# Performance work log

Hardware: AMD Instinct MI355X
Metric: run time of the kernel (lower is better)

Reference implementation:

```python
import jax, jax.numpy as jnp
import numpy as np

# model dims (DeepSeekV2-Lite-like, reduced expert count)
H = 2048      # hidden_dim
NH = 16       # num_heads
NOPE = 128    # qk_nope_head_dim
ROPE = 64     # qk_rope_head_dim (interleaved rotary)
VD = 128      # v_head_dim
QL = 1536     # q_lora_rank
KVL = 512     # kv_lora_rank
E = 8         # num routed experts
TOPK = 2      # num_experts_per_token
MI = 512      # moe_intermediate_dim
SH_I = 2 * MI # num_shared_experts * moe_intermediate_dim
B = 1
S = 2048
T = B * S
EPS = 1e-6
MOE_SCALE = 1.0  # gating_scaling_factor


def setup_inputs() -> dict:
    key = jax.random.key(0)
    ks = jax.random.split(key, 16)
    def w(k, shape):
        return jax.random.normal(k, shape, dtype=jnp.float32) * 0.02
    # interleaved rotary tables: one angle per (even,odd) pair
    half = ROPE // 2
    pos = jnp.arange(S, dtype=jnp.float32)
    inv_freq = 1.0 / (10000.0 ** (jnp.arange(half, dtype=jnp.float32) * 2.0 / ROPE))
    ang = pos[:, None] * inv_freq[None, :]              # [S, half]
    sin = jnp.tile(jnp.sin(ang), (B, 1))                # [T, half]
    cos = jnp.tile(jnp.cos(ang), (B, 1))
    return {
        "x": jax.random.normal(ks[0], (T, H), jnp.float32),
        "skip": jax.random.normal(ks[1], (T, H), jnp.float32),
        "rotary_sin": sin,
        "rotary_cos": cos,
        "ln1_w": jnp.ones((H,), jnp.float32),
        "ln2_w": jnp.ones((H,), jnp.float32),
        "w_qa": w(ks[2], (QL, H)),
        "qa_norm_w": jnp.ones((QL,), jnp.float32),
        "w_qb": w(ks[3], (NH * (NOPE + ROPE), QL)),
        "w_kva": w(ks[4], (KVL + ROPE, H)),
        "kva_norm_w": jnp.ones((KVL,), jnp.float32),
        "w_kb": w(ks[5], (NH * NOPE, KVL)),
        "w_vb": w(ks[6], (NH * VD, KVL)),
        "w_o": w(ks[7], (H, NH * VD)),
        "gate_w": w(ks[8], (E, H)),
        "moe_up_w": w(ks[9], (E, 2 * MI, H)),
        "moe_down_w": w(ks[10], (E, H, MI)),
        "shared_up_w": w(ks[11], (2 * SH_I, H)),
        "shared_down_w": w(ks[12], (H, SH_I)),
        "batch": B,
    }


def _rms(v, w):
    return v * jax.lax.rsqrt(jnp.mean(v * v, axis=-1, keepdims=True) + EPS) * w


def _rope_interleaved(v, sin, cos):
    # v: [T, nh, ROPE]; sin/cos: [T, ROPE//2]; rotate (even, odd) pairs
    x1, x2 = v[..., 0::2], v[..., 1::2]
    s, c = sin[:, None, :], cos[:, None, :]
    o1 = x1 * c - x2 * s
    o2 = x1 * s + x2 * c
    return jnp.stack([o1, o2], axis=-1).reshape(v.shape)


def reference(x, skip, rotary_sin, rotary_cos, ln1_w, ln2_w, w_qa, qa_norm_w,
              w_qb, w_kva, kva_norm_w, w_kb, w_vb, w_o, gate_w,
              moe_up_w, moe_down_w, shared_up_w, shared_down_w, batch):
    Tt = x.shape[0]
    Sq = Tt // batch
    # SkipRMSNorm #1
    x1 = x + skip
    n1 = _rms(x1, ln1_w)
    # ---- MLA attention (prefill path, decoding_batches=0) ----
    qa = _rms(n1 @ w_qa.T, qa_norm_w)                               # [T, QL]
    q = (qa @ w_qb.T).reshape(Tt, NH, NOPE + ROPE)
    q_nope, q_pe = q[..., :NOPE], q[..., NOPE:]
    q_pe = _rope_interleaved(q_pe, rotary_sin, rotary_cos)
    kv = n1 @ w_kva.T                                               # [T, KVL+ROPE]
    ckv = _rms(kv[:, :KVL], kva_norm_w)
    k_pe = _rope_interleaved(kv[:, KVL:][:, None, :], rotary_sin, rotary_cos)  # [T,1,ROPE]
    k_nope = (ckv @ w_kb.T).reshape(Tt, NH, NOPE)
    v = (ckv @ w_vb.T).reshape(Tt, NH, VD)
    qf = jnp.concatenate([q_nope, q_pe], -1).reshape(batch, Sq, NH, NOPE + ROPE)
    kf = jnp.concatenate([k_nope, jnp.broadcast_to(k_pe, (Tt, NH, ROPE))], -1)
    kf = kf.reshape(batch, Sq, NH, NOPE + ROPE)
    vf = v.reshape(batch, Sq, NH, VD)
    scale = 1.0 / np.sqrt(NOPE + ROPE)
    scores = jnp.einsum('bqhd,bkhd->bhqk', qf, kf) * scale
    causal = jnp.tril(jnp.ones((Sq, Sq), bool))
    scores = jnp.where(causal[None, None], scores, jnp.float32(-1e30))
    p = jax.nn.softmax(scores, axis=-1)
    o = jnp.einsum('bhqk,bkhd->bqhd', p, vf).reshape(Tt, NH * VD)
    attn = o @ w_o.T
    # SkipRMSNorm #2
    x2 = x1 + attn
    n2 = _rms(x2, ln2_w)
    # ---- MoE FFN: softmax gate, greedy top-k, normalized probs ----
    probs = jax.nn.softmax(n2 @ gate_w.T, axis=-1)                  # [T, E]
    tv, ti = jax.lax.top_k(probs, TOPK)
    tv = tv / jnp.sum(tv, axis=-1, keepdims=True) * MOE_SCALE
    routed = jnp.zeros_like(n2)
    for e in range(E):  # fixed small expert count; masked dense dispatch
        we = jnp.sum(tv * (ti == e), axis=-1)                       # [T]
        h = n2 @ moe_up_w[e].T                                      # [T, 2*MI]
        h = jax.nn.silu(h[:, :MI]) * h[:, MI:]
        routed = routed + we[:, None] * (h @ moe_down_w[e].T)
    # shared experts (dense swiglu MLP)
    hs = n2 @ shared_up_w.T
    hs = jax.nn.silu(hs[:, :SH_I]) * hs[:, SH_I:]
    ffn = routed + hs @ shared_down_w.T
    return (x2, ffn)
```

## Files before the change

kernel.cpp:

```cpp
#include <hip/hip_runtime.h>
#include <hip/hip_bf16.h>

#define H 2048
#define NH 16
#define NOPE 128
#define ROPE_D 64
#define DQK 192
#define VD 128
#define QL 1536
#define KVL 512
#define NE 8
#define MI_D 512
#define SHI 1024
#define EPS 1e-6f
#define MAXA 5120

typedef unsigned short bfu;
typedef short bf16x8 __attribute__((ext_vector_type(8)));
typedef float f32x4 __attribute__((ext_vector_type(4)));

#define MFMA16(a, b, c) __builtin_amdgcn_mfma_f32_16x16x32_bf16(a, b, c, 0, 0, 0)

#define BAR_PLAIN()   asm volatile("s_barrier" ::: "memory")
#define BAR_LGKM0()   asm volatile("s_waitcnt lgkmcnt(0)\n\ts_barrier" ::: "memory")
#define BAR_VM4()     asm volatile("s_waitcnt vmcnt(4)\n\ts_barrier" ::: "memory")
#define BAR_VM0()     asm volatile("s_waitcnt vmcnt(0)\n\ts_barrier" ::: "memory")

__device__ __forceinline__ float bf2f(bfu u) {
    union { unsigned int i; float f; } w; w.i = ((unsigned int)u) << 16; return w.f;
}
__device__ __forceinline__ bfu f2bf(float f) {
    union { float f; unsigned int i; } u; u.f = f;
    return (bfu)((u.i + 0x7fffu + ((u.i >> 16) & 1u)) >> 16);
}

__device__ __forceinline__ void async16(const bfu* g, bfu* l) {
    __builtin_amdgcn_global_load_lds((const __attribute__((address_space(1))) void*)g,
                                     (__attribute__((address_space(3))) void*)l, 16, 0, 0);
}

__device__ __forceinline__ float blk_sum(float v) {
    __shared__ float sb[4];
    for (int o = 32; o > 0; o >>= 1) v += __shfl_down(v, o, 64);
    int lane = threadIdx.x & 63, w = threadIdx.x >> 6;
    __syncthreads();
    if (lane == 0) sb[w] = v;
    __syncthreads();
    return sb[0] + sb[1] + sb[2] + sb[3];
}

template<int MODE>
__global__ __launch_bounds__(256) void gemm_mfma(const bfu* __restrict__ A, const bfu* __restrict__ B,
                                                 void* __restrict__ Cv, void* __restrict__ Cv2,
                                                 int M, int N, int K, int ldm3,
                                                 const int* __restrict__ aidx,
                                                 const int* __restrict__ eid, long bstride) {
    __shared__ bfu sA[3][128 * 32];
    __shared__ bfu sB[3][128 * 32];
    const int tid = threadIdx.x;
    const int lane = tid & 63, w = tid >> 6;
    const int quad = lane >> 4, li = lane & 15;
    const int m0 = blockIdx.y * 128, n0 = blockIdx.x * 128;
    const bfu* Bp = B + (eid ? (size_t)eid[blockIdx.y] * bstride : 0);

    const int l4 = lane >> 2;
    const int lg = lane & 3;
    const int kc = lg ^ ((lane >> 3) & 3);
    int r0 = m0 + w * 32 + l4, r1 = r0 + 16;
    if (aidx) { r0 = aidx[r0]; r1 = aidx[r1]; }
    const bfu* gA0 = A + (size_t)r0 * K + kc * 8;
    const bfu* gA1 = A + (size_t)r1 * K + kc * 8;
    const bfu* gB0 = Bp + (size_t)(n0 + w * 32 + l4) * K + kc * 8;
    const bfu* gB1 = gB0 + (size_t)16 * K;
    const int oA0 = (w * 32) * 32, oA1 = (w * 32 + 16) * 32;

    const int wm = (w >> 1) * 64, wn = (w & 1) * 64;
    const int fg = (quad ^ ((li >> 1) & 3)) * 8;
    int oa[4], ob[4];
#pragma unroll
    for (int t4 = 0; t4 < 4; ++t4) {
        oa[t4] = (wm + t4 * 16 + li) * 32 + fg;
        ob[t4] = (wn + t4 * 16 + li) * 32 + fg;
    }
    f32x4 acc[4][4];
#pragma unroll
    for (int i = 0; i < 4; ++i)
#pragma unroll
        for (int j = 0; j < 4; ++j) acc[i][j] = (f32x4){0.f, 0.f, 0.f, 0.f};

    const int nb = K / 32;
    async16(gA0, &sA[0][oA0]); async16(gA1, &sA[0][oA1]);
    async16(gB0, &sB[0][oA0]); async16(gB1, &sB[0][oA1]);
    async16(gA0 + 32, &sA[1][oA0]); async16(gA1 + 32, &sA[1][oA1]);
    async16(gB0 + 32, &sB[1][oA0]); async16(gB1 + 32, &sB[1][oA1]);

    int cur = 0;
    for (int it = 0; it < nb; ++it) {
        if (it < nb - 1) { BAR_VM4(); } else { BAR_VM0(); }
        bf16x8 av[4], bv[4];
#pragma unroll
        for (int t4 = 0; t4 < 4; ++t4) av[t4] = *(const bf16x8*)&sA[cur][oa[t4]];
#pragma unroll
        for (int t4 = 0; t4 < 4; ++t4) bv[t4] = *(const bf16x8*)&sB[cur][ob[t4]];
        if (it + 2 < nb) {
            const int k1 = (it + 2) * 32;
            int nxt = cur + 2; if (nxt >= 3) nxt -= 3;
            async16(gA0 + k1, &sA[nxt][oA0]); async16(gA1 + k1, &sA[nxt][oA1]);
            async16(gB0 + k1, &sB[nxt][oA0]); async16(gB1 + k1, &sB[nxt][oA1]);
        }
#pragma unroll
        for (int mt = 0; mt < 4; ++mt)
#pragma unroll
            for (int nt = 0; nt < 4; ++nt)
                acc[mt][nt] = MFMA16(av[mt], bv[nt], acc[mt][nt]);
        if (++cur >= 3) cur = 0;
    }

#pragma unroll
    for (int mt = 0; mt < 4; ++mt)
#pragma unroll
        for (int nt = 0; nt < 4; ++nt) {
            int row = m0 + wm + mt * 16 + quad * 4;
            int col = n0 + wn + nt * 16 + li;
            if (MODE == 0) {
                float* C = (float*)Cv;
#pragma unroll
                for (int r = 0; r < 4; ++r) C[(size_t)(row + r) * N + col] = acc[mt][nt][r];
            } else if (MODE == 1) {
                bfu* C = (bfu*)Cv;
#pragma unroll
                for (int r = 0; r < 4; ++r) C[(size_t)(row + r) * N + col] = f2bf(acc[mt][nt][r]);
            } else {
                if (n0 < 2048) {
                    bfu* C = (bfu*)Cv;
#pragma unroll
                    for (int r = 0; r < 4; ++r) C[(size_t)(row + r) * 2048 + col] = f2bf(acc[mt][nt][r]);
                } else {
                    bfu* C2 = (bfu*)Cv2;
                    ushort4 u;
                    u.x = f2bf(acc[mt][nt][0]); u.y = f2bf(acc[mt][nt][1]);
                    u.z = f2bf(acc[mt][nt][2]); u.w = f2bf(acc[mt][nt][3]);
                    *(ushort4*)(C2 + (size_t)(col - 2048) * ldm3 + row) = u;
                }
            }
        }
}

struct CastArgs {
    const float* s[10];
    bfu* d[10];
    unsigned start[11];
    int pad[10];
};
__global__ __launch_bounds__(256) void k_cast_all(CastArgs a) {
    unsigned g = blockIdx.x * 256 + threadIdx.x;
    if (g >= a.start[10]) return;
    int id = 0;
#pragma unroll
    for (int i = 1; i < 10; ++i) if (g >= a.start[i]) id = i;
    size_t i8 = (size_t)(g - a.start[id]) * 8;
    ushort4 u0 = {0, 0, 0, 0}, u1 = {0, 0, 0, 0};
    if (!a.pad[id] || (i8 >> 11) < 576) {
        const float* s = a.s[id];
        float4 x0 = *(const float4*)(s + i8);
        float4 x1 = *(const float4*)(s + i8 + 4);
        u0.x = f2bf(x0.x); u0.y = f2bf(x0.y); u0.z = f2bf(x0.z); u0.w = f2bf(x0.w);
        u1.x = f2bf(x1.x); u1.y = f2bf(x1.y); u1.z = f2bf(x1.z); u1.w = f2bf(x1.w);
    }
    bfu* d = a.d[id];
    *(ushort4*)(d + i8) = u0;
    *(ushort4*)(d + i8 + 4) = u1;
}

__global__ __launch_bounds__(256) void k_add_rms(const float* __restrict__ x, const float* __restrict__ skip,
                                                 const float* __restrict__ w,
                                                 float* __restrict__ x1, bfu* __restrict__ n1b) {
    int t = blockIdx.x;
    size_t base = (size_t)t * H;
    float loc[8]; float ss = 0.f;
#pragma unroll
    for (int i = 0; i < 8; ++i) {
        int c = threadIdx.x + i * 256;
        float v = x[base + c] + skip[base + c];
        loc[i] = v; ss += v * v;
        x1[base + c] = v;
    }
    float tot = blk_sum(ss);
    float r = rsqrtf(tot / (float)H + EPS);
#pragma unroll
    for (int i = 0; i < 8; ++i) {
        int c = threadIdx.x + i * 256;
        n1b[base + c] = f2bf(loc[i] * r * w[c]);
    }
}

__global__ __launch_bounds__(256) void k_qkv_post(const bfu* __restrict__ qkv,
                                                  const float* __restrict__ qa_nw,
                                                  const float* __restrict__ kva_nw,
                                                  const float* __restrict__ sin_, const float* __restrict__ cos_,
                                                  bfu* __restrict__ qab, bfu* __restrict__ ckv,
                                                  bfu* __restrict__ kpe) {
    int t = blockIdx.x;
    const bfu* row = qkv + (size_t)t * 2176;
    float qa[6]; float ss1 = 0.f;
#pragma unroll
    for (int i = 0; i < 6; ++i) {
        float v = bf2f(row[threadIdx.x + i * 256]); qa[i] = v; ss1 += v * v;
    }
    float v0 = bf2f(row[1536 + threadIdx.x]), v1 = bf2f(row[1792 + threadIdx.x]);
    float s1 = blk_sum(ss1);
    float s2 = blk_sum(v0 * v0 + v1 * v1);
    float r1 = rsqrtf(s1 / (float)QL + EPS);
    float r2 = rsqrtf(s2 / 512.f + EPS);
#pragma unroll
    for (int i = 0; i < 6; ++i) {
        int c = threadIdx.x + i * 256;
        qab[(size_t)t * QL + c] = f2bf(qa[i] * r1 * qa_nw[c]);
    }
    ckv[(size_t)t * 512 + threadIdx.x]       = f2bf(v0 * r2 * kva_nw[threadIdx.x]);
    ckv[(size_t)t * 512 + threadIdx.x + 256] = f2bf(v1 * r2 * kva_nw[threadIdx.x + 256]);
    if (threadIdx.x < 32) {
        int p = threadIdx.x;
        float x1v = bf2f(row[2048 + 2 * p]), x2v = bf2f(row[2048 + 2 * p + 1]);
        float s = sin_[t * 32 + p], c = cos_[t * 32 + p];
        kpe[(size_t)t * 64 + 2 * p]     = f2bf(x1v * c - x2v * s);
        kpe[(size_t)t * 64 + 2 * p + 1] = f2bf(x1v * s + x2v * c);
    }
}

__global__ __launch_bounds__(128) void k_flash_mfma(const bfu* __restrict__ qb,
                                                    const bfu* __restrict__ kn,
                                                    const bfu* __restrict__ kpe,
                                                    const bfu* __restrict__ vt,
                                                    bfu* __restrict__ O,
                                                    const float* __restrict__ rsin,
                                                    const float* __restrict__ rcos, int T) {
    __shared__ bfu Ks[32 * 200];
    __shared__ bfu VtL[128 * 32];
    __shared__ bfu P[32 * 40];
    const int tid = threadIdx.x;
    const int lane = tid & 63, w = tid >> 6;
    const int quad = lane >> 4, li = lane & 15;
    const int q0 = ((int)gridDim.x - 1 - (int)blockIdx.x) * 32;
    const int h = blockIdx.y;
    const float scale = 0.07216878364870322f;

    bf16x8 qf[6];
    {
        int qrow = q0 + w * 16 + li;
        const bfu* qp = qb + ((size_t)qrow * NH + h) * DQK;
#pragma unroll
        for (int s6 = 0; s6 < 6; ++s6) {
            bf16x8 v = *(const bf16x8*)(qp + s6 * 32 + quad * 8);
            if (s6 >= 4) {
                int pb = (s6 - 4) * 16 + quad * 4;
#pragma unroll
                for (int j = 0; j < 4; ++j) {
                    float x1 = bf2f((bfu)v[2 * j]), x2 = bf2f((bfu)v[2 * j + 1]);
                    float s = rsin[qrow * 32 + pb + j], c = rcos[qrow * 32 + pb + j];
                    v[2 * j]     = (short)f2bf(x1 * c - x2 * s);
                    v[2 * j + 1] = (short)f2bf(x1 * s + x2 * c);
                }
            }
            qf[s6] = v;
        }
    }
    f32x4 accO[8];
#pragma unroll
    for (int i = 0; i < 8; ++i) accO[i] = (f32x4){0.f, 0.f, 0.f, 0.f};
    float lrow[4] = {0.f, 0.f, 0.f, 0.f};

    int kr[6], kg[6];
#pragma unroll
    for (int it = 0; it < 6; ++it) { int G = tid + it * 128; kr[it] = G / 24; kg[it] = G % 24; }
    int vn[4], vgl[4], vkc[4];
#pragma unroll
    for (int it = 0; it < 4; ++it) {
        int idx = tid + it * 128; vn[it] = idx >> 2; vgl[it] = idx & 3;
        vkc[it] = vgl[it] ^ ((vn[it] >> 1) & 3);
    }
    bf16x8 kreg[6], vreg[4];
#pragma unroll
    for (int it = 0; it < 6; ++it)
        kreg[it] = (kg[it] < 16) ? *(const bf16x8*)(kn + (size_t)kr[it] * (NH * 128) + h * 128 + kg[it] * 8)
                                 : *(const bf16x8*)(kpe + (size_t)kr[it] * 64 + (kg[it] - 16) * 8);
#pragma unroll
    for (int it = 0; it < 4; ++it)
        vreg[it] = *(const bf16x8*)(vt + (size_t)(h * 128 + vn[it]) * T + vkc[it] * 8);

    const int fgv = (quad ^ ((li >> 1) & 3)) * 8;
    const int kend = q0 + 32;
    for (int k0 = 0; k0 < kend; k0 += 32) {
        BAR_PLAIN();
#pragma unroll
        for (int it = 0; it < 6; ++it) *(bf16x8*)(Ks + kr[it] * 200 + kg[it] * 8) = kreg[it];
#pragma unroll
        for (int it = 0; it < 4; ++it) *(bf16x8*)(VtL + vn[it] * 32 + vgl[it] * 8) = vreg[it];
        if (k0 + 32 < kend) {
            int k1 = k0 + 32;
#pragma unroll
            for (int it = 0; it < 6; ++it)
                kreg[it] = (kg[it] < 16) ? *(const bf16x8*)(kn + (size_t)(k1 + kr[it]) * (NH * 128) + h * 128 + kg[it] * 8)
                                         : *(const bf16x8*)(kpe + (size_t)(k1 + kr[it]) * 64 + (kg[it] - 16) * 8);
#pragma unroll
            for (int it = 0; it < 4; ++it)
                vreg[it] = *(const bf16x8*)(vt + (size_t)(h * 128 + vn[it]) * T + k1 + vkc[it] * 8);
        }
        BAR_LGKM0();
        f32x4 s[2];
#pragma unroll
        for (int ct = 0; ct < 2; ++ct) {
            f32x4 a = (f32x4){0.f, 0.f, 0.f, 0.f};
#pragma unroll
            for (int s6 = 0; s6 < 6; ++s6) {
                bf16x8 kf = *(const bf16x8*)(Ks + (ct * 16 + li) * 200 + s6 * 32 + quad * 8);
                a = MFMA16(qf[s6], kf, a);
            }
            s[ct] = a;
        }
#pragma unroll
        for (int r = 0; r < 4; ++r) {
            int row = q0 + w * 16 + quad * 4 + r;
            float p0 = (k0 + li <= row) ? __expf(s[0][r] * scale) : 0.f;
            float p1 = (k0 + 16 + li <= row) ? __expf(s[1][r] * scale) : 0.f;
            s[0][r] = p0; s[1][r] = p1;
            lrow[r] += p0 + p1;
        }
#pragma unroll
        for (int ct = 0; ct < 2; ++ct)
#pragma unroll
            for (int r = 0; r < 4; ++r)
                P[(w * 16 + quad * 4 + r) * 40 + ct * 16 + li] = f2bf(s[ct][r]);
        bf16x8 pf = *(const bf16x8*)(P + (w * 16 + li) * 40 + quad * 8);
#pragma unroll
        for (int v8 = 0; v8 < 8; ++v8) {
            bf16x8 vf = *(const bf16x8*)(VtL + (v8 * 16 + li) * 32 + fgv);
            accO[v8] = MFMA16(pf, vf, accO[v8]);
        }
    }
#pragma unroll
    for (int r = 0; r < 4; ++r) {
        float l = lrow[r];
        l += __shfl_xor(l, 1); l += __shfl_xor(l, 2);
        l += __shfl_xor(l, 4); l += __shfl_xor(l, 8);
        lrow[r] = 1.0f / l;
    }
#pragma unroll
    for (int v8 = 0; v8 < 8; ++v8)
#pragma unroll
        for (int r = 0; r < 4; ++r) {
            float val = accO[v8][r] * lrow[r];
            O[(size_t)(q0 + w * 16 + quad * 4 + r) * (NH * 128) + h * 128 + v8 * 16 + li] = f2bf(val);
        }
}

__global__ __launch_bounds__(256) void k_x2_n2(const float* __restrict__ x1, const bfu* __restrict__ attn,
                                               const float* __restrict__ ln2w, float* __restrict__ outx2,
                                               bfu* __restrict__ n2b, const float* __restrict__ gw,
                                               int* __restrict__ eidx, float* __restrict__ wts,
                                               int* __restrict__ cnt) {
    int t = blockIdx.x;
    size_t base = (size_t)t * H;
    float loc[8]; float ss = 0.f;
#pragma unroll
    for (int i = 0; i < 8; ++i) {
        int c = threadIdx.x + i * 256;
        float vv = x1[base + c] + bf2f(attn[base + c]);
        loc[i] = vv; ss += vv * vv;
        outx2[base + c] = vv;
    }
    float tot = blk_sum(ss);
    float r = rsqrtf(tot / (float)H + EPS);
    float pe[NE] = {0.f, 0.f, 0.f, 0.f, 0.f, 0.f, 0.f, 0.f};
#pragma unroll
    for (int i = 0; i < 8; ++i) {
        int c = threadIdx.x + i * 256;
        float nv = loc[i] * r * ln2w[c];
        n2b[base + c] = f2bf(nv);
#pragma unroll
        for (int e = 0; e < NE; ++e) pe[e] += nv * gw[e * H + c];
    }
    __shared__ float logits[NE];
    for (int e = 0; e < NE; ++e) {
        float tt = blk_sum(pe[e]);
        if (threadIdx.x == 0) logits[e] = tt;
    }
    __syncthreads();
    if (threadIdx.x == 0) {
        float m = logits[0];
        for (int e = 1; e < NE; ++e) m = fmaxf(m, logits[e]);
        float p[NE];
        for (int e = 0; e < NE; ++e) p[e] = __expf(logits[e] - m);
        int i1 = 0;
        for (int e = 1; e < NE; ++e) if (p[e] > p[i1]) i1 = e;
        int i2 = -1;
        for (int e = 0; e < NE; ++e) if (e != i1 && (i2 < 0 || p[e] > p[i2])) i2 = e;
        float denom = p[i1] + p[i2];
        eidx[t * 2] = i1; eidx[t * 2 + 1] = i2;
        wts[t * 2] = p[i1] / denom; wts[t * 2 + 1] = p[i2] / denom;
        atomicAdd(&cnt[i1], 1); atomicAdd(&cnt[i2], 1);
    }
}

__global__ __launch_bounds__(256) void k_moe_init(int* __restrict__ cnt, int* __restrict__ slot,
                                                  int* __restrict__ eid, int* __restrict__ idx,
                                                  float* __restrict__ aw) {
    int tid = threadIdx.x;
    if (tid < NE) { cnt[tid] = 0; slot[tid] = 0; }
    if (tid < 40) eid[tid] = 0;
    for (int i = tid; i < MAXA; i += 256) { idx[i] = 0; aw[i] = 0.f; }
}

__global__ __launch_bounds__(64) void k_moe_scan(const int* __restrict__ cnt, int* __restrict__ base,
                                                 int* __restrict__ eid) {
    if (threadIdx.x == 0) {
        int off = 0;
        for (int e = 0; e < NE; ++e) {
            base[e] = off;
            int nb = (cnt[e] + 127) >> 7;
            for (int j = 0; j < nb; ++j) eid[(off >> 7) + j] = e;
            off += nb << 7;
        }
    }
}

__global__ __launch_bounds__(256) void k_moe_scatter(const int* __restrict__ eidx, const float* __restrict__ wts,
                                                     const int* __restrict__ base, int* __restrict__ slot,
                                                     int* __restrict__ idx, float* __restrict__ aw,
                                                     int* __restrict__ posmap) {
    int t = blockIdx.x * 256 + threadIdx.x;
#pragma unroll
    for (int j = 0; j < 2; ++j) {
        int e = eidx[t * 2 + j];
        int p = base[e] + atomicAdd(&slot[e], 1);
        idx[p] = t; aw[p] = wts[t * 2 + j]; posmap[t * 2 + j] = p;
    }
}

__global__ __launch_bounds__(256) void k_silu_sparse(const bfu* __restrict__ hb, const float* __restrict__ aw,
                                                     bfu* __restrict__ g) {
    int row = blockIdx.x;
    float we = aw[row];
    const bfu* hr = hb + (size_t)row * 1024;
    bfu* gr = g + (size_t)row * 512;
#pragma unroll
    for (int j = 0; j < 2; ++j) {
        int i = threadIdx.x + j * 256;
        float a = bf2f(hr[i]), b = bf2f(hr[512 + i]);
        gr[i] = f2bf(we * a / (1.0f + __expf(-a)) * b);
    }
}

__global__ __launch_bounds__(256) void k_silu_sh(const bfu* __restrict__ hb, bfu* __restrict__ g) {
    int t = blockIdx.x;
    const bfu* row = hb + (size_t)t * 2048;
    bfu* grow = g + (size_t)t * 1024;
#pragma unroll
    for (int j = 0; j < 4; ++j) {
        int i = threadIdx.x + j * 256;
        float a = bf2f(row[i]), b = bf2f(row[1024 + i]);
        grow[i] = f2bf(a / (1.0f + __expf(-a)) * b);
    }
}

__global__ __launch_bounds__(256) void k_ffn_out(const float* __restrict__ routed, const bfu* __restrict__ dsp,
                                                 const int* __restrict__ posmap, float* __restrict__ out,
                                                 size_t TH) {
    int t = blockIdx.x;
    int p1 = posmap[t * 2], p2 = posmap[t * 2 + 1];
    const bfu* d1 = dsp + (size_t)p1 * H;
    const bfu* d2 = dsp + (size_t)p2 * H;
#pragma unroll
    for (int j = 0; j < 8; ++j) {
        int c = threadIdx.x + j * 256;
        out[TH + (size_t)t * H + c] = routed[(size_t)t * H + c] + bf2f(d1[c]) + bf2f(d2[c]);
    }
}

extern "C" void kernel_launch(void* const* d_in, const int* in_sizes, int n_in,
                              void* d_out, int out_size, void* d_ws, size_t ws_size,
                              hipStream_t stream) {
    const float* x      = (const float*)d_in[0];
    const float* skip   = (const float*)d_in[1];
    const float* rsin   = (const float*)d_in[2];
    const float* rcos   = (const float*)d_in[3];
    const float* ln1w   = (const float*)d_in[4];
    const float* ln2w   = (const float*)d_in[5];
    const float* w_qa   = (const float*)d_in[6];
    const float* qa_nw  = (const float*)d_in[7];
    const float* w_qb   = (const float*)d_in[8];
    const float* w_kva  = (const float*)d_in[9];
    const float* kva_nw = (const float*)d_in[10];
    const float* w_kb   = (const float*)d_in[11];
    const float* w_vb   = (const float*)d_in[12];
    const float* w_o    = (const float*)d_in[13];
    const float* gate_w = (const float*)d_in[14];
    const float* mup    = (const float*)d_in[15];
    const float* mdown  = (const float*)d_in[16];
    const float* shup   = (const float*)d_in[17];
    const float* shdown = (const float*)d_in[18];

    const int T = in_sizes[0] / H;

    bfu* WB = (bfu*)d_ws;
    bfu* wqkv_b  = WB + 0;
    bfu* wkbv_b  = WB + 4456448;
    bfu* wqb_b   = WB + 6553600;
    bfu* wo_b    = WB + 11272192;
    bfu* mup_b   = WB + 15466496;
    bfu* mdown_b = WB + 32243712;
    bfu* shup_b  = WB + 40632320;
    bfu* shdn_b  = WB + 44826624;
    const size_t WBYTES = 93847552;

    char* AB = (char*)d_ws + WBYTES;
    float* x1f    = (float*)(AB + 0);
    float* routed = (float*)(AB + 0);
    bfu*   n1b    = (bfu*)(AB + 16777216);
    bfu*   qkvb   = (bfu*)(AB + 25165824);
    bfu*   knb    = (bfu*)(AB + 25165824);
    bfu*   hsp    = (bfu*)(AB + 25165824);
    bfu*   qab    = (bfu*)(AB + 35651584);
    bfu*   gsp    = (bfu*)(AB + 35651584);
    bfu*   qbb    = (bfu*)(AB + 41943040);
    bfu*   attnb  = (bfu*)(AB + 41943040);
    bfu*   ckvb   = (bfu*)(AB + 54525952);
    bfu*   kpeb   = (bfu*)(AB + 56623104);
    char*  G      = AB + 56885248;
    int*   eidx   = (int*)(G);
    float* wts    = (float*)(G + 16384);
    int*   posmap = (int*)(G + 32768);
    int*   midx   = (int*)(G + 49152);
    float* maw    = (float*)(G + 69632);
    int*   mcnt   = (int*)(G + 90112);
    int*   mbase  = (int*)(G + 90112 + 64);
    int*   mslot  = (int*)(G + 90112 + 128);
    int*   meid   = (int*)(G + 90112 + 192);
    bfu*   ob     = (bfu*)(AB + 57016320);
    bfu*   gsb    = (bfu*)(AB + 57016320);
    bfu*   vtb    = (bfu*)(AB + 65404928);
    bfu*   hsb    = (bfu*)(AB + 65404928);
    bfu*   dsp    = (bfu*)(AB + 65404928);
    const size_t REQ = WBYTES + 86376448;
    if (ws_size < REQ) return;

    {
        CastArgs ca;
        const float* ss[10] = {w_qa, w_kva, w_kb, w_vb, w_qb, w_o, mup, mdown, shup, shdown};
        bfu* dd[10] = {wqkv_b, wqkv_b + 3145728, wkbv_b, wkbv_b + 1048576, wqb_b,
                       wo_b, mup_b, mdown_b, shup_b, shdn_b};
        unsigned n8[10] = {393216, 163840, 131072, 131072, 589824, 524288, 2097152, 1048576, 524288, 262144};
        unsigned acc = 0;
        for (int i = 0; i < 10; ++i) { ca.s[i] = ss[i]; ca.d[i] = dd[i]; ca.start[i] = acc; acc += n8[i]; ca.pad[i] = (i == 1); }
        ca.start[10] = acc;
        k_cast_all<<<22912, 256, 0, stream>>>(ca);
    }

    k_add_rms<<<T, 256, 0, stream>>>(x, skip, ln1w, x1f, n1b);
    gemm_mfma<1><<<dim3(2176 / 128, T / 128), 256, 0, stream>>>(n1b, wqkv_b, qkvb, nullptr, T, 2176, H, 0, nullptr, nullptr, 0);
    k_qkv_post<<<T, 256, 0, stream>>>(qkvb, qa_nw, kva_nw, rsin, rcos, qab, ckvb, kpeb);
    gemm_mfma<1><<<dim3((NH * DQK) / 128, T / 128), 256, 0, stream>>>(qab, wqb_b, qbb, nullptr, T, NH * DQK, QL, 0, nullptr, nullptr, 0);
    gemm_mfma<4><<<dim3(4096 / 128, T / 128), 256, 0, stream>>>(ckvb, wkbv_b, knb, vtb, T, 4096, KVL, T, nullptr, nullptr, 0);
    k_flash_mfma<<<dim3(T / 32, NH), 128, 0, stream>>>(qbb, knb, kpeb, vtb, ob, rsin, rcos, T);
    gemm_mfma<1><<<dim3(H / 128, T / 128), 256, 0, stream>>>(ob, wo_b, attnb, nullptr, T, H, NH * VD, 0, nullptr, nullptr, 0);
    k_moe_init<<<1, 256, 0, stream>>>(mcnt, mslot, meid, midx, maw);
    k_x2_n2<<<T, 256, 0, stream>>>(x1f, attnb, ln2w, (float*)d_out, n1b, gate_w, eidx, wts, mcnt);
    k_moe_scan<<<1, 64, 0, stream>>>(mcnt, mbase, meid);
    k_moe_scatter<<<T / 256, 256, 0, stream>>>(eidx, wts, mbase, mslot, midx, maw, posmap);
    gemm_mfma<1><<<dim3(2048 / 128, T / 128), 256, 0, stream>>>(n1b, shup_b, hsb, nullptr, T, 2048, H, 0, nullptr, nullptr, 0);
    k_silu_sh<<<T, 256, 0, stream>>>(hsb, gsb);
    gemm_mfma<0><<<dim3(H / 128, T / 128), 256, 0, stream>>>(gsb, shdn_b, routed, nullptr, T, H, SHI, 0, nullptr, nullptr, 0);
    gemm_mfma<1><<<dim3(1024 / 128, MAXA / 128), 256, 0, stream>>>(
        n1b, mup_b, hsp, nullptr, MAXA, 1024, H, 0, midx, meid, (long)1024 * H);
    k_silu_sparse<<<MAXA, 256, 0, stream>>>(hsp, maw, gsp);
    gemm_mfma<1><<<dim3(H / 128, MAXA / 128), 256, 0, stream>>>(
        gsp, mdown_b, dsp, nullptr, MAXA, H, MI_D, 0, nullptr, meid, (long)H * MI_D);
    k_ffn_out<<<T, 256, 0, stream>>>(routed, dsp, posmap, (float*)d_out, (size_t)T * H);
}
```

Baseline: 677.4 us.

## Batch independent GEMMs into single grouped launches and merge SiLU kernels

Replaces the templated GEMM with a runtime-mode grouped kernel that runs two independent GEMM problems in one 1-D grid: q_b with kv_b, shared-up with MoE-up, and shared-down with MoE-down. The two SiLU kernels are also merged into one launch. This cuts launch count and fills the GPU better when one problem alone leaves CUs idle or has a tail. In exchange the output mode becomes a runtime branch instead of a compile-time template, which may cost registers and add epilogue branching.

```diff
diff --git a/kernel.cpp b/kernel.cpp
--- a/kernel.cpp
+++ b/kernel.cpp
@@ -49,19 +49,27 @@
     return sb[0] + sb[1] + sb[2] + sb[3];
 }
 
-template<int MODE>
-__global__ __launch_bounds__(256) void gemm_mfma(const bfu* __restrict__ A, const bfu* __restrict__ B,
-                                                 void* __restrict__ Cv, void* __restrict__ Cv2,
-                                                 int M, int N, int K, int ldm3,
-                                                 const int* __restrict__ aidx,
-                                                 const int* __restrict__ eid, long bstride) {
-    __shared__ bfu sA[3][128 * 32];
-    __shared__ bfu sB[3][128 * 32];
+struct GemmSeg {
+    const bfu* A; const bfu* B; void* C; void* C2;
+    const int* aidx; const int* eid;
+    long bstride;
+    int N, K, ldm3, mode, nx, ntiles;
+};
+
+__device__ __forceinline__ void gemm_body(const bfu* __restrict__ A, const bfu* __restrict__ B,
+                                          void* __restrict__ Cv, void* __restrict__ Cv2,
+                                          int N, int K, int ldm3, int mode,
+                                          const int* __restrict__ aidx,
+                                          const int* __restrict__ eid, long bstride,
+                                          int bx, int by,
+                                          bfu* sAb, bfu* sBb) {
+    bfu (*sA)[128 * 32] = (bfu (*)[128 * 32])sAb;
+    bfu (*sB)[128 * 32] = (bfu (*)[128 * 32])sBb;
     const int tid = threadIdx.x;
     const int lane = tid & 63, w = tid >> 6;
     const int quad = lane >> 4, li = lane & 15;
-    const int m0 = blockIdx.y * 128, n0 = blockIdx.x * 128;
-    const bfu* Bp = B + (eid ? (size_t)eid[blockIdx.y] * bstride : 0);
+    const int m0 = by * 128, n0 = bx * 128;
+    const bfu* Bp = B + (eid ? (size_t)eid[by] * bstride : 0);
 
     const int l4 = lane >> 2;
     const int lg = lane & 3;
@@ -122,11 +130,11 @@
         for (int nt = 0; nt < 4; ++nt) {
             int row = m0 + wm + mt * 16 + quad * 4;
             int col = n0 + wn + nt * 16 + li;
-            if (MODE == 0) {
+            if (mode == 0) {
                 float* C = (float*)Cv;
 #pragma unroll
                 for (int r = 0; r < 4; ++r) C[(size_t)(row + r) * N + col] = acc[mt][nt][r];
-            } else if (MODE == 1) {
+            } else if (mode == 1) {
                 bfu* C = (bfu*)Cv;
 #pragma unroll
                 for (int r = 0; r < 4; ++r) C[(size_t)(row + r) * N + col] = f2bf(acc[mt][nt][r]);
@@ -144,6 +152,20 @@
                 }
             }
         }
+}
+
+__global__ __launch_bounds__(256) void gemm_multi(GemmSeg s0, GemmSeg s1) {
+    __shared__ bfu sA[3][128 * 32];
+    __shared__ bfu sB[3][128 * 32];
+    int b = blockIdx.x;
+    if (b < s0.ntiles) {
+        gemm_body(s0.A, s0.B, s0.C, s0.C2, s0.N, s0.K, s0.ldm3, s0.mode,
+                  s0.aidx, s0.eid, s0.bstride, b % s0.nx, b / s0.nx, &sA[0][0], &sB[0][0]);
+    } else {
+        int lb = b - s0.ntiles;
+        gemm_body(s1.A, s1.B, s1.C, s1.C2, s1.N, s1.K, s1.ldm3, s1.mode,
+                  s1.aidx, s1.eid, s1.bstride, lb % s1.nx, lb / s1.nx, &sA[0][0], &sB[0][0]);
+    }
 }
 
 struct CastArgs {
@@ -437,29 +459,30 @@
     }
 }
 
-__global__ __launch_bounds__(256) void k_silu_sparse(const bfu* __restrict__ hb, const float* __restrict__ aw,
-                                                     bfu* __restrict__ g) {
-    int row = blockIdx.x;
-    float we = aw[row];
-    const bfu* hr = hb + (size_t)row * 1024;
-    bfu* gr = g + (size_t)row * 512;
-#pragma unroll
-    for (int j = 0; j < 2; ++j) {
-        int i = threadIdx.x + j * 256;
-        float a = bf2f(hr[i]), b = bf2f(hr[512 + i]);
-        gr[i] = f2bf(we * a / (1.0f + __expf(-a)) * b);
-    }
-}
-
-__global__ __launch_bounds__(256) void k_silu_sh(const bfu* __restrict__ hb, bfu* __restrict__ g) {
-    int t = blockIdx.x;
-    const bfu* row = hb + (size_t)t * 2048;
-    bfu* grow = g + (size_t)t * 1024;
-#pragma unroll
-    for (int j = 0; j < 4; ++j) {
-        int i = threadIdx.x + j * 256;
-        float a = bf2f(row[i]), b = bf2f(row[1024 + i]);
-        grow[i] = f2bf(a / (1.0f + __expf(-a)) * b);
+__global__ __launch_bounds__(256) void k_silu_both(const bfu* __restrict__ hsh, bfu* __restrict__ gsh,
+                                                   const bfu* __restrict__ hsp, const float* __restrict__ aw,
+                                                   bfu* __restrict__ gsp, int T) {
+    int b = blockIdx.x;
+    if (b < T) {
+        const bfu* row = hsh + (size_t)b * 2048;
+        bfu* grow = gsh + (size_t)b * 1024;
+#pragma unroll
+        for (int j = 0; j < 4; ++j) {
+            int i = threadIdx.x + j * 256;
+            float a = bf2f(row[i]), bb = bf2f(row[1024 + i]);
+            grow[i] = f2bf(a / (1.0f + __expf(-a)) * bb);
+        }
+    } else {
+        int row = b - T;
+        float we = aw[row];
+        const bfu* hr = hsp + (size_t)row * 1024;
+        bfu* gr = gsp + (size_t)row * 512;
+#pragma unroll
+        for (int j = 0; j < 2; ++j) {
+            int i = threadIdx.x + j * 256;
+            float a = bf2f(hr[i]), bb = bf2f(hr[512 + i]);
+            gr[i] = f2bf(we * a / (1.0f + __expf(-a)) * bb);
+        }
     }
 }
 
@@ -475,6 +498,15 @@
         int c = threadIdx.x + j * 256;
         out[TH + (size_t)t * H + c] = routed[(size_t)t * H + c] + bf2f(d1[c]) + bf2f(d2[c]);
     }
+}
+
+static inline GemmSeg mk_seg(const bfu* A, const bfu* B, void* C, void* C2,
+                             const int* aidx, const int* eid, long bstride,
+                             int N, int K, int ldm3, int mode, int nx, int ny) {
+    GemmSeg s;
+    s.A = A; s.B = B; s.C = C; s.C2 = C2; s.aidx = aidx; s.eid = eid; s.bstride = bstride;
+    s.N = N; s.K = K; s.ldm3 = ldm3; s.mode = mode; s.nx = nx; s.ntiles = nx * ny;
+    return s;
 }
 
 extern "C" void kernel_launch(void* const* d_in, const int* in_sizes, int n_in,
@@ -557,23 +589,35 @@
     }
 
     k_add_rms<<<T, 256, 0, stream>>>(x, skip, ln1w, x1f, n1b);
-    gemm_mfma<1><<<dim3(2176 / 128, T / 128), 256, 0, stream>>>(n1b, wqkv_b, qkvb, nullptr, T, 2176, H, 0, nullptr, nullptr, 0);
+    {
+        GemmSeg s = mk_seg(n1b, wqkv_b, qkvb, nullptr, nullptr, nullptr, 0, 2176, H, 0, 1, 2176 / 128, T / 128);
+        gemm_multi<<<s.ntiles, 256, 0, stream>>>(s, s);
+    }
     k_qkv_post<<<T, 256, 0, stream>>>(qkvb, qa_nw, kva_nw, rsin, rcos, qab, ckvb, kpeb);
-    gemm_mfma<1><<<dim3((NH * DQK) / 128, T / 128), 256, 0, stream>>>(qab, wqb_b, qbb, nullptr, T, NH * DQK, QL, 0, nullptr, nullptr, 0);
-    gemm_mfma<4><<<dim3(4096 / 128, T / 128), 256, 0, stream>>>(ckvb, wkbv_b, knb, vtb, T, 4096, KVL, T, nullptr, nullptr, 0);
+    {
+        GemmSeg sq = mk_seg(qab, wqb_b, qbb, nullptr, nullptr, nullptr, 0, NH * DQK, QL, 0, 1, (NH * DQK) / 128, T / 128);
+        GemmSeg sk = mk_seg(ckvb, wkbv_b, knb, vtb, nullptr, nullptr, 0, 4096, KVL, T, 4, 4096 / 128, T / 128);
+        gemm_multi<<<sq.ntiles + sk.ntiles, 256, 0, stream>>>(sq, sk);
+    }
     k_flash_mfma<<<dim3(T / 32, NH), 128, 0, stream>>>(qbb, knb, kpeb, vtb, ob, rsin, rcos, T);
-    gemm_mfma<1><<<dim3(H / 128, T / 128), 256, 0, stream>>>(ob, wo_b, attnb, nullptr, T, H, NH * VD, 0, nullptr, nullptr, 0);
+    {
+        GemmSeg s = mk_seg(ob, wo_b, attnb, nullptr, nullptr, nullptr, 0, H, NH * VD, 0, 1, H / 128, T / 128);
+        gemm_multi<<<s.ntiles, 256, 0, stream>>>(s, s);
+    }
     k_moe_init<<<1, 256, 0, stream>>>(mcnt, mslot, meid, midx, maw);
     k_x2_n2<<<T, 256, 0, stream>>>(x1f, attnb, ln2w, (float*)d_out, n1b, gate_w, eidx, wts, mcnt);
     k_moe_scan<<<1, 64, 0, stream>>>(mcnt, mbase, meid);
     k_moe_scatter<<<T / 256, 256, 0, stream>>>(eidx, wts, mbase, mslot, midx, maw, posmap);
-    gemm_mfma<1><<<dim3(2048 / 128, T / 128), 256, 0, stream>>>(n1b, shup_b, hsb, nullptr, T, 2048, H, 0, nullptr, nullptr, 0);
-    k_silu_sh<<<T, 256, 0, stream>>>(hsb, gsb);
-    gemm_mfma<0><<<dim3(H / 128, T / 128), 256, 0, stream>>>(gsb, shdn_b, routed, nullptr, T, H, SHI, 0, nullptr, nullptr, 0);
-    gemm_mfma<1><<<dim3(1024 / 128, MAXA / 128), 256, 0, stream>>>(
-        n1b, mup_b, hsp, nullptr, MAXA, 1024, H, 0, midx, meid, (long)1024 * H);
-    k_silu_sparse<<<MAXA, 256, 0, stream>>>(hsp, maw, gsp);
-    gemm_mfma<1><<<dim3(H / 128, MAXA / 128), 256, 0, stream>>>(
-        gsp, mdown_b, dsp, nullptr, MAXA, H, MI_D, 0, nullptr, meid, (long)H * MI_D);
+    {
+        GemmSeg ssh = mk_seg(n1b, shup_b, hsb, nullptr, nullptr, nullptr, 0, 2048, H, 0, 1, 2048 / 128, T / 128);
+        GemmSeg smo = mk_seg(n1b, mup_b, hsp, nullptr, midx, meid, (long)1024 * H, 1024, H, 0, 1, 1024 / 128, MAXA / 128);
+        gemm_multi<<<ssh.ntiles + smo.ntiles, 256, 0, stream>>>(ssh, smo);
+    }
+    k_silu_both<<<T + MAXA, 256, 0, stream>>>(hsb, gsb, hsp, maw, gsp, T);
+    {
+        GemmSeg ssd = mk_seg(gsb, shdn_b, routed, nullptr, nullptr, nullptr, 0, H, SHI, 0, 0, H / 128, T / 128);
+        GemmSeg smd = mk_seg(gsp, mdown_b, dsp, nullptr, nullptr, meid, (long)H * MI_D, H, MI_D, 0, 1, H / 128, MAXA / 128);
+        gemm_multi<<<ssd.ntiles + smd.ntiles, 256, 0, stream>>>(ssd, smd);
+    }
     k_ffn_out<<<T, 256, 0, stream>>>(routed, dsp, posmap, (float*)d_out, (size_t)T * H);
 }
```

New measurement: 650.4 us. 1.04x faster.
